# Kernel tuning notes

Measured on AMD Instinct MI355X. Metric: run time of the kernel, lower is better.

Reference implementation:

```python
import jax, jax.numpy as jnp
import numpy as np

BETA = 0.25
DECAY = 0.99
EPS = 1e-05
K = 1024        # num_codebook_vectors
D = 256         # latent_dim


def setup_inputs() -> dict:
    key = jax.random.key(0)
    k1, k2, k3 = jax.random.split(key, 3)
    return {
        "z": jax.random.normal(k1, (32, D, 32, 32), dtype=jnp.float32),
        "embedding": jax.random.normal(k2, (K, D), dtype=jnp.float32),
        "ema_cluster_size": jnp.zeros((K,), dtype=jnp.float32),
        "ema_w": jax.random.normal(k3, (K, D), dtype=jnp.float32),
    }


def reference(z, embedding, ema_cluster_size, ema_w):
    B, C, H, W = z.shape
    zp = jnp.transpose(z, (0, 2, 3, 1))            # [B,H,W,C]
    zf = zp.reshape(-1, C)                          # [N, D], N = B*H*W

    # squared L2 distances: ||z||^2 + ||e||^2 - 2 z e^T  -> [N, K]
    d = (jnp.sum(zf * zf, axis=1, keepdims=True)
         + jnp.sum(embedding * embedding, axis=1)
         - 2.0 * (zf @ embedding.T))
    idx = jnp.argmin(d, axis=1)                     # [N]

    # one-hot @ embedding == gather of codebook rows
    z_q = embedding[idx].reshape(zp.shape)          # [B,H,W,C]

    # EMA codebook update (training branch)
    counts = jnp.zeros((K,), dtype=zf.dtype).at[idx].add(1.0)   # encodings.sum(0)
    cs = ema_cluster_size * DECAY + (1.0 - DECAY) * counts
    n = jnp.sum(cs)
    cs = (cs + EPS) / (n + K * EPS) * n             # Laplace smoothing
    dw = jax.ops.segment_sum(zf, idx, num_segments=K)           # encodings.T @ zf
    new_ema_w = ema_w * DECAY + (1.0 - DECAY) * dw
    new_embedding = new_ema_w / cs[:, None]

    # commitment loss + straight-through estimator
    e_latent_loss = jnp.mean((jax.lax.stop_gradient(z_q) - zp) ** 2)
    loss = BETA * e_latent_loss
    z_q_st = zp + jax.lax.stop_gradient(z_q - zp)
    z_q_out = jnp.transpose(z_q_st, (0, 3, 1, 2))   # [B,C,H,W]

    return z_q_out, idx[:, None], loss, new_embedding, cs, new_ema_w
```

## Files before the change

### kernel.cpp

```cpp
#include <hip/hip_runtime.h>

typedef unsigned long long ull;
typedef __attribute__((ext_vector_type(8))) short bf16x8;
typedef __attribute__((ext_vector_type(4))) float f32x4;
typedef __attribute__((ext_vector_type(8))) unsigned short u16x8;

#define DECAY 0.99f
#define BETA 0.25f
#define EPSV 1e-5f
#define EPSGAP 0.0625f

#define Dd 256
#define Kk 1024
#define Nn 32768
#define ZELEM 8388608

__device__ __forceinline__ unsigned short f2bf(float f) {
    unsigned int x = __float_as_uint(f);
    x += 0x7FFFu + ((x >> 16) & 1u);
    return (unsigned short)(x >> 16);
}
__device__ __forceinline__ float bf2f(unsigned short b) {
    return __uint_as_float(((unsigned int)b) << 16);
}
__device__ __forceinline__ unsigned mono(unsigned b) {
    return b ^ (((int)b >> 31) | 0x80000000u);
}
__device__ __forceinline__ float unmono(unsigned m) {
    unsigned b = (m & 0x80000000u) ? (m ^ 0x80000000u) : ~m;
    return __uint_as_float(b);
}
__device__ __forceinline__ unsigned umin32(unsigned a, unsigned b) { return a < b ? a : b; }
__device__ __forceinline__ unsigned umax32(unsigned a, unsigned b) { return a > b ? a : b; }

__global__ __launch_bounds__(256) void prep_e_kernel(
        const float* __restrict__ emb, unsigned short* __restrict__ ehg,
        unsigned short* __restrict__ elg, float* __restrict__ esq,
        int* __restrict__ hist, int* __restrict__ flagcnt,
        float* __restrict__ loss_fix, float* __restrict__ dw) {
    const int nsub = blockIdx.x;
    const int t = threadIdx.x;
    if (t < 16) hist[nsub * 16 + t] = 0;
    if (nsub == 0 && t == 16) flagcnt[0] = 0;
    if (nsub == 0 && t == 17) loss_fix[0] = 0.0f;
    {
        float4* dwp = (float4*)dw;
        #pragma unroll
        for (int j = 0; j < 4; ++j)
            dwp[(size_t)(nsub * 256 + t) * 4 + j] = make_float4(0.f, 0.f, 0.f, 0.f);
    }
    #pragma unroll
    for (int it = 0; it < 2; ++it) {
        const int item = it * 256 + t;
        const int kc = item >> 6, lane = item & 63;
        const int quad = lane >> 4, nl = lane & 15;
        const float* ep = emb + (size_t)(nsub * 16 + nl) * Dd + kc * 32 + quad * 8;
        const float4 a = *(const float4*)ep;
        const float4 b4 = *(const float4*)(ep + 4);
        const float v[8] = {a.x, a.y, a.z, a.w, b4.x, b4.y, b4.z, b4.w};
        u16x8 hi, lo;
        #pragma unroll
        for (int j = 0; j < 8; ++j) {
            const unsigned short h = f2bf(v[j]);
            hi[j] = h;
            lo[j] = f2bf(v[j] - bf2f(h));
        }
        const size_t off = ((size_t)(nsub * 8 + kc) * 64 + lane) * 8;
        *(u16x8*)&ehg[off] = hi;
        *(u16x8*)&elg[off] = lo;
    }
    {
        const int nl = t >> 4, seg = t & 15;
        const float* ep = emb + (size_t)(nsub * 16 + nl) * Dd + seg * 16;
        float s = 0.0f;
        #pragma unroll
        for (int j = 0; j < 4; ++j) {
            const float4 v4 = *(const float4*)(ep + j * 4);
            s += v4.x * v4.x + v4.y * v4.y + v4.z * v4.z + v4.w * v4.w;
        }
        #pragma unroll
        for (int d = 1; d < 16; d <<= 1) s += __shfl_xor(s, d);
        if (seg == 0) esq[nsub * 16 + nl] = s;
    }
}

__global__ __launch_bounds__(256) void dist_kernel(
        const float* __restrict__ z, const unsigned short* __restrict__ ehg,
        const unsigned short* __restrict__ elg, const float* __restrict__ esq,
        const float* __restrict__ emb,
        float* __restrict__ zq, float* __restrict__ dw,
        int* __restrict__ idx_i, float* __restrict__ idx_f,
        int* __restrict__ hist, int* __restrict__ flagcnt,
        int* __restrict__ flaglist, float* __restrict__ flagval,
        float* __restrict__ loss_p) {
    __shared__ __align__(16) unsigned char smem[70656];
    __shared__ int kidx[64];
    unsigned short* zh = (unsigned short*)smem;
    unsigned short* zl = (unsigned short*)(smem + 32768);
    ull* mb   = (ull*)(smem + 65536);
    ull* ms   = (ull*)(smem + 67584);
    float* zsqp = (float*)(smem + 69632);
    float* eldsf = (float*)smem;

    const int t = threadIdx.x, w = t >> 6, L = t & 63;
    const int quad = L >> 4, lr = L & 15;
    const int m0 = blockIdx.x * 64;
    const int b = m0 >> 10, hw0 = m0 & 1023;

    {
        const int c0 = w * 64;
        const float* zp = z + (size_t)b * 262144 + hw0 + L;
        float s = 0.0f;
        #pragma unroll
        for (int cg = 0; cg < 8; ++cg) {
            float v[8];
            #pragma unroll
            for (int j = 0; j < 8; ++j)
                v[j] = zp[(size_t)(c0 + cg * 8 + j) * 1024];
            u16x8 hi, lo;
            #pragma unroll
            for (int j = 0; j < 8; ++j) {
                s = fmaf(v[j], v[j], s);
                const unsigned short h = f2bf(v[j]);
                hi[j] = h;
                lo[j] = f2bf(v[j] - bf2f(h));
            }
            const int chunk = ((c0 >> 3) + cg) ^ (L & 7);
            *(u16x8*)&zh[L * 256 + chunk * 8] = hi;
            *(u16x8*)&zl[L * 256 + chunk * 8] = lo;
        }
        zsqp[L * 4 + w] = s;
    }
    __syncthreads();

    const unsigned short* ehw = ehg + (size_t)(w * 1024 + L) * 8;
    const unsigned short* elw = elg + (size_t)(w * 1024 + L) * 8;

    unsigned bb[16], ss[16];
    #pragma unroll
    for (int i = 0; i < 16; ++i) { bb[i] = 0xFFFFFFFFu; ss[i] = 0xFFFFFFFFu; }

    bf16x8 Bh[2][2], Bl[2][2];
    #pragma unroll
    for (int ni = 0; ni < 2; ++ni) {
        Bh[0][ni] = *(const bf16x8*)(ehw + (size_t)ni * 4096);
        Bl[0][ni] = *(const bf16x8*)(elw + (size_t)ni * 4096);
    }
    bf16x8 Ah[2][4], Al[2][4];
    #pragma unroll
    for (int mi = 0; mi < 4; ++mi) {
        const int chunk = quad ^ (lr & 7);
        const int o = (mi * 16 + lr) * 256 + chunk * 8;
        Ah[0][mi] = *(const bf16x8*)&zh[o];
        Al[0][mi] = *(const bf16x8*)&zl[o];
    }

    for (int nt = 0; nt < 8; ++nt) {
        f32x4 acc[4][2];
        #pragma unroll
        for (int mi = 0; mi < 4; ++mi)
            #pragma unroll
            for (int ni = 0; ni < 2; ++ni) acc[mi][ni] = (f32x4){0.f, 0.f, 0.f, 0.f};

        #pragma unroll
        for (int kc = 0; kc < 8; ++kc) {
            const int cur = kc & 1, nxt = cur ^ 1;
            const int nkc = (kc + 1) & 7;
            const int nnt = (kc == 7) ? ((nt + 1) & 7) : nt;
            #pragma unroll
            for (int ni = 0; ni < 2; ++ni) {
                const size_t o = (size_t)nnt * 32768 + (size_t)ni * 4096 + (size_t)nkc * 512;
                Bh[nxt][ni] = *(const bf16x8*)(ehw + o);
                Bl[nxt][ni] = *(const bf16x8*)(elw + o);
            }
            #pragma unroll
            for (int mi = 0; mi < 4; ++mi) {
                const int chunk = (nkc * 4 + quad) ^ (lr & 7);
                const int o = (mi * 16 + lr) * 256 + chunk * 8;
                Ah[nxt][mi] = *(const bf16x8*)&zh[o];
                Al[nxt][mi] = *(const bf16x8*)&zl[o];
            }
            __builtin_amdgcn_s_setprio(1);
            #pragma unroll
            for (int mi = 0; mi < 4; ++mi)
                #pragma unroll
                for (int ni = 0; ni < 2; ++ni) {
                    acc[mi][ni] = __builtin_amdgcn_mfma_f32_16x16x32_bf16(Ah[cur][mi], Bh[cur][ni], acc[mi][ni], 0, 0, 0);
                    acc[mi][ni] = __builtin_amdgcn_mfma_f32_16x16x32_bf16(Ah[cur][mi], Bl[cur][ni], acc[mi][ni], 0, 0, 0);
                    acc[mi][ni] = __builtin_amdgcn_mfma_f32_16x16x32_bf16(Al[cur][mi], Bh[cur][ni], acc[mi][ni], 0, 0, 0);
                }
            __builtin_amdgcn_s_setprio(0);
        }
        const int q0 = nt * 8 + w * 2;
        const float e0b = esq[q0 * 16 + lr] + 512.0f;
        const float e1b = esq[(q0 + 1) * 16 + lr] + 512.0f;
        #pragma unroll
        for (int mi = 0; mi < 4; ++mi)
            #pragma unroll
            for (int reg = 0; reg < 4; ++reg) {
                const int i = mi * 4 + reg;
                #pragma unroll
                for (int ni = 0; ni < 2; ++ni) {
                    const float val = fmaf(-2.0f, acc[mi][ni][reg], ni ? e1b : e0b);
                    const unsigned pk = (__float_as_uint(val) & 0xFFFFFFC0u) | (unsigned)(q0 + ni);
                    const unsigned mx = umax32(bb[i], pk);
                    bb[i] = umin32(bb[i], pk);
                    ss[i] = umin32(ss[i], mx);
                }
            }
    }

    #pragma unroll
    for (int mi = 0; mi < 4; ++mi)
        #pragma unroll
        for (int reg = 0; reg < 4; ++reg) {
            const int i = mi * 4 + reg;
            ull b2 = ((ull)(bb[i] & 0xFFFFFFC0u) << 14) | (ull)((bb[i] & 63u) * 16 + lr);
            ull s2 = ((ull)(ss[i] & 0xFFFFFFC0u) << 14) | (ull)((ss[i] & 63u) * 16 + lr);
            #pragma unroll
            for (int d = 1; d < 16; d <<= 1) {
                const ull ob = __shfl_xor(b2, d);
                const ull os = __shfl_xor(s2, d);
                const ull mx = ob < b2 ? b2 : ob;
                b2 = ob < b2 ? ob : b2;
                const ull ns = os < s2 ? os : s2;
                s2 = mx < ns ? mx : ns;
            }
            if (lr == 0) {
                const int row = mi * 16 + quad * 4 + reg;
                mb[w * 64 + row] = b2;
                ms[w * 64 + row] = s2;
            }
        }
    __syncthreads();

    if (t < 64) {
        ull b2 = mb[t], s2 = ms[t];
        #pragma unroll
        for (int ww = 1; ww < 4; ++ww) {
            const ull ob = mb[ww * 64 + t], os = ms[ww * 64 + t];
            const ull mx = ob < b2 ? b2 : ob;
            b2 = ob < b2 ? ob : b2;
            const ull ns = os < s2 ? os : s2;
            s2 = mx < ns ? mx : ns;
        }
        const int k = (int)(b2 & 16383ull);
        const float v1 = __uint_as_float((unsigned)(b2 >> 14)) - 512.0f;
        const float v2 = __uint_as_float((unsigned)(s2 >> 14)) - 512.0f;
        idx_i[m0 + t] = k;
        idx_f[m0 + t] = (float)k;
        kidx[t] = k;
        atomicAdd(&hist[k], 1);
        if (v2 - v1 < EPSGAP) {
            const int pos = atomicAdd(flagcnt, 1);
            flaglist[pos] = m0 + t;
            flagval[pos] = v1;
        }
        float lp = v1 + zsqp[t * 4] + zsqp[t * 4 + 1] + zsqp[t * 4 + 2] + zsqp[t * 4 + 3];
        #pragma unroll
        for (int d = 32; d > 0; d >>= 1) lp += __shfl_down(lp, d);
        if (t == 0) loss_p[blockIdx.x] = lp;
    }
    __syncthreads();

    {
        const int c = t;
        const int ch = c >> 3, cj = c & 7;
        #pragma unroll 4
        for (int p = 0; p < 64; ++p) {
            const int a = p * 256 + ((ch ^ (p & 7)) << 3) + cj;
            const float v = bf2f(zh[a]) + bf2f(zl[a]);
            atomicAdd(&dw[(size_t)kidx[p] * Dd + c], v);
        }
    }
    __syncthreads();

    for (int pr = w; pr < 64; pr += 4) {
        const float* er = emb + (size_t)kidx[pr] * Dd;
        #pragma unroll
        for (int g = 0; g < 4; ++g)
            eldsf[pr * 257 + g * 64 + L] = er[g * 64 + L];
    }
    __syncthreads();

    {
        const int g = t & 15;
        const int cl = t >> 4;
        float* zqb = zq + (size_t)b * 262144 + hw0 + g * 4;
        #pragma unroll
        for (int pass = 0; pass < 16; ++pass) {
            const int c = pass * 16 + cl;
            float4 v;
            v.x = eldsf[(g * 4 + 0) * 257 + c];
            v.y = eldsf[(g * 4 + 1) * 257 + c];
            v.z = eldsf[(g * 4 + 2) * 257 + c];
            v.w = eldsf[(g * 4 + 3) * 257 + c];
            *(float4*)(zqb + (size_t)c * 1024) = v;
        }
    }
}

__global__ __launch_bounds__(256) void fixup_kernel(
        const float* __restrict__ z, const float* __restrict__ emb,
        const float* __restrict__ esq, const int* __restrict__ flagcnt,
        const int* __restrict__ flaglist, const float* __restrict__ flagval,
        int* __restrict__ idx_i, float* __restrict__ idx_f,
        int* __restrict__ hist, float* __restrict__ loss_fix,
        float* __restrict__ zq, float* __restrict__ dw) {
    __shared__ float zrow[256];
    __shared__ ull red[256];
    __shared__ int s_pair[2];
    const int t = threadIdx.x;
    const int total = flagcnt[0];
    for (int fi = blockIdx.x; fi < total; fi += 512) {
        const int n = flaglist[fi];
        const int b = n >> 10, hw = n & 1023;
        __syncthreads();
        zrow[t] = z[(size_t)b * 262144 + (size_t)t * 1024 + hw];
        __syncthreads();
        ull best = ~0ull;
        #pragma unroll
        for (int kc = 0; kc < 4; ++kc) {
            const int k = t * 4 + kc;
            const float* ep = emb + (size_t)k * Dd;
            float dot = 0.0f;
            #pragma unroll 8
            for (int c4 = 0; c4 < 64; ++c4) {
                const float4 e4 = *(const float4*)(ep + c4 * 4);
                const float4 z4 = *(const float4*)&zrow[c4 * 4];
                dot = fmaf(z4.x, e4.x, dot);
                dot = fmaf(z4.y, e4.y, dot);
                dot = fmaf(z4.z, e4.z, dot);
                dot = fmaf(z4.w, e4.w, dot);
            }
            const float val = esq[k] - 2.0f * dot;
            const ull pk = ((ull)mono(__float_as_uint(val)) << 32) | (unsigned)k;
            if (pk < best) best = pk;
        }
        red[t] = best;
        __syncthreads();
        for (int s = 128; s > 0; s >>= 1) {
            if (t < s) { if (red[t + s] < red[t]) red[t] = red[t + s]; }
            __syncthreads();
        }
        if (t == 0) {
            const int knew = (int)(unsigned)(red[0] & 0xFFFFFFFFull);
            const float vnew = unmono((unsigned)(red[0] >> 32));
            const int kold = idx_i[n];
            s_pair[0] = kold;
            s_pair[1] = knew;
            if (knew != kold) {
                idx_i[n] = knew;
                idx_f[n] = (float)knew;
                atomicSub(&hist[kold], 1);
                atomicAdd(&hist[knew], 1);
            }
            atomicAdd(loss_fix, vnew - flagval[fi]);
        }
        __syncthreads();
        const int kold = s_pair[0], knew = s_pair[1];
        if (knew != kold) {
            const float zv = zrow[t];
            atomicAdd(&dw[(size_t)kold * Dd + t], -zv);
            atomicAdd(&dw[(size_t)knew * Dd + t], zv);
            zq[(size_t)b * 262144 + (size_t)t * 1024 + hw] = emb[(size_t)knew * Dd + t];
        }
    }
}

__global__ void scan_fin1_kernel(const int* __restrict__ hist,
                                 const float* __restrict__ ema_cs,
                                 const float* __restrict__ loss_p,
                                 const float* __restrict__ loss_fix,
                                 float* __restrict__ cs_out,
                                 float* __restrict__ loss_out) {
    __shared__ float wred[16], wred2[16];
    const int t = threadIdx.x;
    const int w = t >> 6, lane = t & 63;
    const int v = hist[t];
    const float csr = ema_cs[t] * DECAY + (1.0f - DECAY) * (float)v;
    float r = csr;
    float r2 = (t < 512) ? loss_p[t] : 0.0f;
    #pragma unroll
    for (int d = 32; d > 0; d >>= 1) { r += __shfl_xor(r, d); r2 += __shfl_xor(r2, d); }
    if (lane == 0) { wred[w] = r; wred2[w] = r2; }
    __syncthreads();
    if (t < 16) {
        float rr = wred[t], rr2 = wred2[t];
        #pragma unroll
        for (int d = 1; d < 16; d <<= 1) { rr += __shfl_xor(rr, d); rr2 += __shfl_xor(rr2, d); }
        if (t == 0) { wred[0] = rr; wred2[0] = rr2; }
    }
    __syncthreads();
    const float nsum = wred[0];
    const float cs = (csr + EPSV) / (nsum + (float)Kk * EPSV) * nsum;
    cs_out[t] = cs;
    if (t == 0) loss_out[0] = BETA * (wred2[0] + loss_fix[0]) / (float)ZELEM;
}

__global__ __launch_bounds__(256) void finalize2_kernel(
        const float* __restrict__ ema_w, const float* __restrict__ dw,
        const float* __restrict__ cs_out,
        float* __restrict__ new_emb_out, float* __restrict__ new_ema_w_out) {
    const int i = blockIdx.x * 256 + threadIdx.x;
    const float nw = ema_w[i] * DECAY + (1.0f - DECAY) * dw[i];
    const float cs = cs_out[i >> 8];
    new_ema_w_out[i] = nw;
    new_emb_out[i]   = nw / cs;
}

extern "C" void kernel_launch(void* const* d_in, const int* in_sizes, int n_in,
                              void* d_out, int out_size, void* d_ws, size_t ws_size,
                              hipStream_t stream) {
    const float* z      = (const float*)d_in[0];
    const float* emb    = (const float*)d_in[1];
    const float* ema_cs = (const float*)d_in[2];
    const float* ema_w  = (const float*)d_in[3];

    float* out = (float*)d_out;
    float* zq_out        = out;
    float* idx_out_f     = out + 8388608;
    float* loss_out      = out + 8421376;
    float* new_emb_out   = out + 8421377;
    float* cs_out        = out + 8683521;
    float* new_ema_w_out = out + 8684545;

    int*   idx_i    = (int*)d_ws;
    int*   flagcnt  = idx_i + 32768;
    float* loss_fix = (float*)(flagcnt + 16);
    int*   flaglist = (int*)(loss_fix + 16);
    float* flagval  = (float*)(flaglist + 32768);
    int*   hist     = (int*)(flagval + 32768);
    float* esq      = (float*)(hist + 1024);
    float* loss_p   = esq + 1024;
    unsigned short* ehg = (unsigned short*)(loss_p + 512);
    unsigned short* elg = ehg + 262144;

    float* dw = new_emb_out;

    prep_e_kernel<<<64, 256, 0, stream>>>(emb, ehg, elg, esq, hist, flagcnt,
                                          loss_fix, dw);
    dist_kernel<<<Nn / 64, 256, 0, stream>>>(z, ehg, elg, esq, emb, zq_out, dw,
                                             idx_i, idx_out_f, hist, flagcnt,
                                             flaglist, flagval, loss_p);
    fixup_kernel<<<512, 256, 0, stream>>>(z, emb, esq, flagcnt, flaglist,
                                          flagval, idx_i, idx_out_f, hist,
                                          loss_fix, zq_out, dw);
    scan_fin1_kernel<<<1, 1024, 0, stream>>>(hist, ema_cs, loss_p, loss_fix,
                                             cs_out, loss_out);
    finalize2_kernel<<<Kk * Dd / 256, 256, 0, stream>>>(ema_w, dw, cs_out,
                                                        new_emb_out, new_ema_w_out);
}
```

Baseline: 245.3 us.

## Replicate dw accumulator across workspace copies to cut atomic contention

The segment-sum accumulator dw moves from the output buffer into up to 8 replicas in workspace, sized to the available workspace. Each block picks a replica by blockIdx, and finalize2 sums the replicas. The scatter now reads z columns straight from global memory after the zq store instead of the bf16 hi/lo pair in LDS, and zeroing is done with hipMemsetAsync instead of inside prep_e. This aims to reduce same-address atomic contention on popular codewords, at the cost of extra memset and reduction traffic. Fixup still writes to replica 0, which remains correct because finalize2 sums all replicas.

```diff
diff --git a/kernel.cpp b/kernel.cpp
--- a/kernel.cpp
+++ b/kernel.cpp
@@ -37,18 +37,12 @@
         const float* __restrict__ emb, unsigned short* __restrict__ ehg,
         unsigned short* __restrict__ elg, float* __restrict__ esq,
         int* __restrict__ hist, int* __restrict__ flagcnt,
-        float* __restrict__ loss_fix, float* __restrict__ dw) {
+        float* __restrict__ loss_fix) {
     const int nsub = blockIdx.x;
     const int t = threadIdx.x;
     if (t < 16) hist[nsub * 16 + t] = 0;
     if (nsub == 0 && t == 16) flagcnt[0] = 0;
     if (nsub == 0 && t == 17) loss_fix[0] = 0.0f;
-    {
-        float4* dwp = (float4*)dw;
-        #pragma unroll
-        for (int j = 0; j < 4; ++j)
-            dwp[(size_t)(nsub * 256 + t) * 4 + j] = make_float4(0.f, 0.f, 0.f, 0.f);
-    }
     #pragma unroll
     for (int it = 0; it < 2; ++it) {
         const int item = it * 256 + t;
@@ -88,7 +82,7 @@
         const float* __restrict__ z, const unsigned short* __restrict__ ehg,
         const unsigned short* __restrict__ elg, const float* __restrict__ esq,
         const float* __restrict__ emb,
-        float* __restrict__ zq, float* __restrict__ dw,
+        float* __restrict__ zq, float* __restrict__ dwr, int repmask,
         int* __restrict__ idx_i, float* __restrict__ idx_f,
         int* __restrict__ hist, int* __restrict__ flagcnt,
         int* __restrict__ flaglist, float* __restrict__ flagval,
@@ -263,18 +257,6 @@
     }
     __syncthreads();
 
-    {
-        const int c = t;
-        const int ch = c >> 3, cj = c & 7;
-        #pragma unroll 4
-        for (int p = 0; p < 64; ++p) {
-            const int a = p * 256 + ((ch ^ (p & 7)) << 3) + cj;
-            const float v = bf2f(zh[a]) + bf2f(zl[a]);
-            atomicAdd(&dw[(size_t)kidx[p] * Dd + c], v);
-        }
-    }
-    __syncthreads();
-
     for (int pr = w; pr < 64; pr += 4) {
         const float* er = emb + (size_t)kidx[pr] * Dd;
         #pragma unroll
@@ -296,6 +278,16 @@
             v.z = eldsf[(g * 4 + 2) * 257 + c];
             v.w = eldsf[(g * 4 + 3) * 257 + c];
             *(float4*)(zqb + (size_t)c * 1024) = v;
+        }
+    }
+
+    {
+        const int c = t;
+        const float* zcol = z + (size_t)b * 262144 + (size_t)c * 1024 + hw0;
+        float* dwb = dwr + (size_t)(blockIdx.x & repmask) * (Kk * Dd);
+        #pragma unroll 4
+        for (int p = 0; p < 64; ++p) {
+            atomicAdd(&dwb[(size_t)kidx[p] * Dd + c], zcol[p]);
         }
     }
 }
@@ -399,11 +391,13 @@
 }
 
 __global__ __launch_bounds__(256) void finalize2_kernel(
-        const float* __restrict__ ema_w, const float* __restrict__ dw,
-        const float* __restrict__ cs_out,
+        const float* __restrict__ ema_w, const float* __restrict__ dwr,
+        int nrep, const float* __restrict__ cs_out,
         float* __restrict__ new_emb_out, float* __restrict__ new_ema_w_out) {
     const int i = blockIdx.x * 256 + threadIdx.x;
-    const float nw = ema_w[i] * DECAY + (1.0f - DECAY) * dw[i];
+    float s = 0.0f;
+    for (int r = 0; r < nrep; ++r) s += dwr[(size_t)r * (Kk * Dd) + i];
+    const float nw = ema_w[i] * DECAY + (1.0f - DECAY) * s;
     const float cs = cs_out[i >> 8];
     new_ema_w_out[i] = nw;
     new_emb_out[i]   = nw / cs;
@@ -435,19 +429,26 @@
     float* loss_p   = esq + 1024;
     unsigned short* ehg = (unsigned short*)(loss_p + 512);
     unsigned short* elg = ehg + 262144;
-
-    float* dw = new_emb_out;
-
+    size_t dwr_off = ((size_t)((char*)(elg + 262144) - (char*)d_ws) + 255) & ~(size_t)255;
+    float* dwr = (float*)((char*)d_ws + dwr_off);
+    const size_t repbytes = (size_t)Kk * Dd * 4;
+    size_t rem = (ws_size > dwr_off) ? ws_size - dwr_off : 0;
+    int nrep = 1;
+    while (nrep < 8 && (size_t)(nrep * 2) * repbytes <= rem) nrep <<= 1;
+
+    hipMemsetAsync(dwr, 0, (size_t)nrep * repbytes, stream);
     prep_e_kernel<<<64, 256, 0, stream>>>(emb, ehg, elg, esq, hist, flagcnt,
-                                          loss_fix, dw);
-    dist_kernel<<<Nn / 64, 256, 0, stream>>>(z, ehg, elg, esq, emb, zq_out, dw,
-                                             idx_i, idx_out_f, hist, flagcnt,
-                                             flaglist, flagval, loss_p);
+                                          loss_fix);
+    dist_kernel<<<Nn / 64, 256, 0, stream>>>(z, ehg, elg, esq, emb, zq_out,
+                                             dwr, nrep - 1, idx_i, idx_out_f,
+                                             hist, flagcnt, flaglist, flagval,
+                                             loss_p);
     fixup_kernel<<<512, 256, 0, stream>>>(z, emb, esq, flagcnt, flaglist,
                                           flagval, idx_i, idx_out_f, hist,
-                                          loss_fix, zq_out, dw);
+                                          loss_fix, zq_out, dwr);
     scan_fin1_kernel<<<1, 1024, 0, stream>>>(hist, ema_cs, loss_p, loss_fix,
                                              cs_out, loss_out);
-    finalize2_kernel<<<Kk * Dd / 256, 256, 0, stream>>>(ema_w, dw, cs_out,
-                                                        new_emb_out, new_ema_w_out);
-}
+    finalize2_kernel<<<Kk * Dd / 256, 256, 0, stream>>>(ema_w, dwr, nrep,
+                                                        cs_out, new_emb_out,
+                                                        new_ema_w_out);
+}
```

Measured after the change: 237.0 us. 1.03x faster.
